# Kernel tuning notes

Hardware: AMD Instinct MI355X
Metric: run time of the kernel (lower is better)

Reference implementation:

```python
import jax, jax.numpy as jnp
import numpy as np

B, T, C, H = 2, 2048, 2048, 16
DH = C // H  # 128
INNER = 4 * C  # 8192
EPS = 1e-5


def _ln(x, w, b):
    mu = jnp.mean(x, axis=-1, keepdims=True)
    var = jnp.mean((x - mu) ** 2, axis=-1, keepdims=True)
    return (x - mu) * jax.lax.rsqrt(var + EPS) * w + b


def _apply_rotary(x, cos, sin):
    # x: [B,H,T,DH]; cos/sin: [T,DH//2] broadcast over B,H
    x1 = x[..., ::2]
    x2 = x[..., 1::2]
    r = jnp.stack([x1 * cos - x2 * sin, x1 * sin + x2 * cos], axis=-1)
    return r.reshape(r.shape[:-2] + (-1,))


def setup_inputs() -> dict:
    key = jax.random.key(0)
    ks = jax.random.split(key, 8)
    std = 0.02
    x = jax.random.normal(ks[0], (B, T, C), dtype=jnp.float32)
    # RoPE tables
    inv_freq = 1.0 / (10000.0 ** (np.arange(0, DH, 2, dtype=np.float32) / DH))
    ang = np.arange(T, dtype=np.float32)[:, None] * inv_freq[None, :]  # [T, DH//2]
    cos = jnp.asarray(np.cos(ang))
    sin = jnp.asarray(np.sin(ang))
    return {
        "x": x,
        "cos": cos,
        "sin": sin,
        "ln1_w": jnp.ones((C,), jnp.float32),
        "ln1_b": jnp.zeros((C,), jnp.float32),
        "ln2_w": jnp.ones((C,), jnp.float32),
        "ln2_b": jnp.zeros((C,), jnp.float32),
        "W_qkv": jax.random.normal(ks[1], (C, 3 * C), jnp.float32) * std,
        "W_o": jax.random.normal(ks[2], (C, C), jnp.float32) * std,
        "W1": jax.random.normal(ks[3], (C, INNER), jnp.float32) * std,
        "W2": jax.random.normal(ks[4], (C, INNER), jnp.float32) * std,
        "W3": jax.random.normal(ks[5], (INNER, C), jnp.float32) * std,
    }


def reference(x, cos, sin, ln1_w, ln1_b, ln2_w, ln2_b, W_qkv, W_o, W1, W2, W3):
    # --- attention sub-block (pre-LN) ---
    a = _ln(x, ln1_w, ln1_b)
    qkv = a @ W_qkv  # [B,T,3C]
    q, k, v = jnp.split(qkv, 3, axis=-1)
    q = q.reshape(B, T, H, DH).transpose(0, 2, 1, 3)  # [B,H,T,DH]
    k = k.reshape(B, T, H, DH).transpose(0, 2, 1, 3)
    v = v.reshape(B, T, H, DH).transpose(0, 2, 1, 3)
    q = _apply_rotary(q, cos, sin)
    k = _apply_rotary(k, cos, sin)
    scores = jnp.einsum("bhtd,bhsd->bhts", q, k) / jnp.sqrt(jnp.float32(DH))
    mask = jnp.triu(jnp.full((T, T), -jnp.inf, dtype=scores.dtype), k=1)
    scores = scores + mask
    attn = jax.nn.softmax(scores, axis=-1)
    y = jnp.einsum("bhts,bhsd->bhtd", attn, v)
    y = y.transpose(0, 2, 1, 3).reshape(B, T, C) @ W_o
    x = x + y
    # --- SwiGLU MLP sub-block (pre-LN) ---
    h = _ln(x, ln2_w, ln2_b)
    m = (jax.nn.silu(h @ W1) * (h @ W2)) @ W3
    return x + m
```

## Files before the change

kernel.cpp:

```cpp
#include <hip/hip_runtime.h>
#include <hip/hip_bf16.h>
#include <cstdint>

#define DEVINL __device__ __forceinline__

using f32x4  = __attribute__((ext_vector_type(4))) float;
using short8 = __attribute__((ext_vector_type(8))) short;
using short4v = __attribute__((ext_vector_type(4))) short;

DEVINL float bf2f(__hip_bfloat16 h){ return __bfloat162float(h); }
DEVINL __hip_bfloat16 f2bf(float f){ return __float2bfloat16(f); }
DEVINL short bfbits(float f){ __hip_bfloat16 h = __float2bfloat16(f); short s; __builtin_memcpy(&s, &h, 2); return s; }
DEVINL float sb2f(short s){ uint32_t u = ((uint32_t)(uint16_t)s) << 16; float f; __builtin_memcpy(&f, &u, 4); return f; }

DEVINL void gl_lds16(const void* g, void* l){
  __builtin_amdgcn_global_load_lds((const __attribute__((address_space(1))) void*)g,
                                   (__attribute__((address_space(3))) void*)l, 16, 0, 0);
}

__global__ __launch_bounds__(256) void wtrans(const float* __restrict__ src,
                                              __hip_bfloat16* __restrict__ dst,
                                              int R, int C){
  __shared__ float tile[32][33];
  const int tr0 = blockIdx.y*32, tc0 = blockIdx.x*32;
  const int t = threadIdx.x;
  const int lr = t >> 3, lc = (t & 7) * 4;
  float4 v = *(const float4*)(src + (size_t)(tr0+lr)*C + tc0 + lc);
  tile[lr][lc] = v.x; tile[lr][lc+1] = v.y; tile[lr][lc+2] = v.z; tile[lr][lc+3] = v.w;
  __syncthreads();
  short4v o;
  o[0] = bfbits(tile[lc+0][lr]);
  o[1] = bfbits(tile[lc+1][lr]);
  o[2] = bfbits(tile[lc+2][lr]);
  o[3] = bfbits(tile[lc+3][lr]);
  *(short4v*)(dst + (size_t)(tc0+lr)*R + tr0 + lc) = o;
}

__global__ __launch_bounds__(256) void ln_k(const float* __restrict__ x,
                                            const float* __restrict__ w,
                                            const float* __restrict__ bia,
                                            __hip_bfloat16* __restrict__ out){
  const int row = blockIdx.x, t = threadIdx.x;
  const float* xr = x + (size_t)row*2048;
  float4 v0 = *(const float4*)(xr + t*4);
  float4 v1 = *(const float4*)(xr + 1024 + t*4);
  float s  = v0.x+v0.y+v0.z+v0.w + v1.x+v1.y+v1.z+v1.w;
  float ss = v0.x*v0.x+v0.y*v0.y+v0.z*v0.z+v0.w*v0.w
           + v1.x*v1.x+v1.y*v1.y+v1.z*v1.z+v1.w*v1.w;
  #pragma unroll
  for (int o=1;o<64;o<<=1){ s += __shfl_xor(s,o); ss += __shfl_xor(ss,o); }
  __shared__ float red[8];
  const int wv = t>>6, ln = t&63;
  if (ln==0){ red[wv]=s; red[4+wv]=ss; }
  __syncthreads();
  s = red[0]+red[1]+red[2]+red[3]; ss = red[4]+red[5]+red[6]+red[7];
  const float mu = s*(1.f/2048.f);
  const float inv = rsqrtf(ss*(1.f/2048.f) - mu*mu + 1e-5f);
  {
    float4 wv4 = *(const float4*)(w + t*4);
    float4 bv4 = *(const float4*)(bia + t*4);
    short4v o;
    o[0]=bfbits((v0.x-mu)*inv*wv4.x + bv4.x);
    o[1]=bfbits((v0.y-mu)*inv*wv4.y + bv4.y);
    o[2]=bfbits((v0.z-mu)*inv*wv4.z + bv4.z);
    o[3]=bfbits((v0.w-mu)*inv*wv4.w + bv4.w);
    *(short4v*)(out + (size_t)row*2048 + t*4) = o;
  }
  {
    float4 wv4 = *(const float4*)(w + 1024 + t*4);
    float4 bv4 = *(const float4*)(bia + 1024 + t*4);
    short4v o;
    o[0]=bfbits((v1.x-mu)*inv*wv4.x + bv4.x);
    o[1]=bfbits((v1.y-mu)*inv*wv4.y + bv4.y);
    o[2]=bfbits((v1.z-mu)*inv*wv4.z + bv4.z);
    o[3]=bfbits((v1.w-mu)*inv*wv4.w + bv4.w);
    *(short4v*)(out + (size_t)row*2048 + 1024 + t*4) = o;
  }
}

template<int EPI, int BM>
__global__ __launch_bounds__(512, 2) void gemm256(
    const __hip_bfloat16* __restrict__ A,
    const __hip_bfloat16* __restrict__ Bt,
    __hip_bfloat16* __restrict__ Cb,
    float* __restrict__ Cf,
    const float* __restrict__ resid,
    const __hip_bfloat16* __restrict__ emul,
    int M, int N, int K, int NTN)
{
  constexpr int MF     = BM/32;
  constexpr int NA     = BM/64;
  constexpr int ABYTES = BM*128;
  constexpr int TILEB  = ABYTES + 32768;
  constexpr int NLD    = NA + 4;
  extern __shared__ char smem[];
  const int tid = threadIdx.x, lane = tid & 63, wave = tid >> 6;
  const int l15 = lane & 15, l4 = lane >> 4;
  const int wm = wave >> 2, wn = wave & 3;

  const int nwg = gridDim.x;
  const int id  = blockIdx.x;
  const int swz = (id & 7) * (nwg >> 3) + (id >> 3);
  const int by = swz / NTN, bx = swz % NTN;
  const int row0 = by * BM, col0 = bx * 256;

  const __hip_bfloat16* gptr[NLD];
  int ldsoff[NLD];
  #pragma unroll
  for (int g = 0; g < NLD; ++g){
    const int gg = (g < NA) ? g : g - NA;
    const int r    = gg*64 + (tid >> 3);
    const int colp = (tid & 7) * 16;
    const int coll = colp ^ ((r & 7) << 4);
    if (g < NA) gptr[g] = A  + (size_t)(row0 + r)*K + (coll >> 1);
    else        gptr[g] = Bt + (size_t)(col0 + r)*K + (coll >> 1);
    ldsoff[g] = (g < NA ? 0 : ABYTES) + gg*8192 + tid*16;
  }
  auto STAGE = [&](int bufc, int ktile){
    #pragma unroll
    for (int g = 0; g < NLD; ++g)
      gl_lds16(gptr[g] + (size_t)ktile*64, smem + bufc + ldsoff[g]);
  };

  const int swzm = (l15 & 7) << 4;
  const int aRow = (wm*(BM/2) + l15) * 128;
  const int bRow = ABYTES + (wn*64 + l15) * 128;
  const int colT0 = (l4*16) ^ swzm;
  const int colT1 = (64 + l4*16) ^ swzm;

  f32x4 acc[MF][4] = {};
  const int NT = K >> 6;

  STAGE(0, 0);
  STAGE(TILEB, 1);
  __builtin_amdgcn_sched_barrier(0);
  if constexpr (BM == 256) asm volatile("s_waitcnt vmcnt(8)" ::: "memory");
  else                     asm volatile("s_waitcnt vmcnt(6)" ::: "memory");
  __builtin_amdgcn_s_barrier();
  __builtin_amdgcn_sched_barrier(0);

  for (int t = 0; t < NT; ++t){
    const int bufc = (t & 1) * TILEB;
    #pragma unroll
    for (int ks = 0; ks < 2; ++ks){
      const int ct = (ks == 0) ? colT0 : colT1;
      short8 a[MF], b[4];
      #pragma unroll
      for (int m = 0; m < MF; ++m) a[m] = *(const short8*)(smem + bufc + aRow + m*2048 + ct);
      #pragma unroll
      for (int n = 0; n < 4; ++n) b[n] = *(const short8*)(smem + bufc + bRow + n*2048 + ct);
      __builtin_amdgcn_s_setprio(1);
      #pragma unroll
      for (int m = 0; m < MF; ++m)
        #pragma unroll
        for (int n = 0; n < 4; ++n)
          acc[m][n] = __builtin_amdgcn_mfma_f32_16x16x32_bf16(a[m], b[n], acc[m][n], 0, 0, 0);
      __builtin_amdgcn_s_setprio(0);
    }
    __builtin_amdgcn_sched_barrier(0);
    __builtin_amdgcn_s_barrier();
    __builtin_amdgcn_sched_barrier(0);
    if (t + 2 < NT){
      STAGE(bufc, t + 2);
      __builtin_amdgcn_sched_barrier(0);
      if constexpr (BM == 256) asm volatile("s_waitcnt vmcnt(8)" ::: "memory");
      else                     asm volatile("s_waitcnt vmcnt(6)" ::: "memory");
    } else {
      asm volatile("s_waitcnt vmcnt(0)" ::: "memory");
    }
    __builtin_amdgcn_s_barrier();
    __builtin_amdgcn_sched_barrier(0);
  }

  #pragma unroll
  for (int m = 0; m < MF; ++m){
    const int r0 = row0 + wm*(BM/2) + m*16 + l4*4;
    #pragma unroll
    for (int n = 0; n < 4; ++n){
      const int c = col0 + wn*64 + n*16 + l15;
      #pragma unroll
      for (int j = 0; j < 4; ++j){
        const size_t idx = (size_t)(r0 + j)*N + c;
        const float v = acc[m][n][j];
        if constexpr (EPI == 1)      Cf[idx] = v + resid[idx];
        else if constexpr (EPI == 2) Cb[idx] = f2bf(v / (1.f + __expf(-v)));
        else if constexpr (EPI == 3) Cb[idx] = f2bf(v * bf2f(emul[idx]));
        else                         Cb[idx] = f2bf(v);
      }
    }
  }
}

__global__ __launch_bounds__(256) void ropepack(
    const __hip_bfloat16* __restrict__ qkv, const float* __restrict__ cosT, const float* __restrict__ sinT,
    __hip_bfloat16* __restrict__ Qo, __hip_bfloat16* __restrict__ Ko, __hip_bfloat16* __restrict__ Vo)
{
  __shared__ short vt[128][72];
  const int bh = blockIdx.y, b = bh>>4, h = bh&15;
  const int t0 = blockIdx.x*64, tid = threadIdx.x;
  const int tr = tid>>2, q4 = tid&3;
  const int tg = t0 + tr;
  const __hip_bfloat16* base = qkv + ((size_t)(b*2048 + tg))*6144 + h*128;
  const int pp0 = q4*16;
  float cs[16], sn[16];
  #pragma unroll
  for (int i=0;i<4;i++){
    float4 c4 = *(const float4*)(cosT + (size_t)tg*64 + pp0 + i*4);
    float4 s4 = *(const float4*)(sinT + (size_t)tg*64 + pp0 + i*4);
    cs[i*4+0]=c4.x; cs[i*4+1]=c4.y; cs[i*4+2]=c4.z; cs[i*4+3]=c4.w;
    sn[i*4+0]=s4.x; sn[i*4+1]=s4.y; sn[i*4+2]=s4.z; sn[i*4+3]=s4.w;
  }
  #pragma unroll
  for (int qk=0; qk<2; ++qk){
    const __hip_bfloat16* src = base + qk*2048;
    __hip_bfloat16* dst = (qk==0 ? Qo : Ko) + ((size_t)bh*2048 + tg)*128 + pp0*2;
    short8 ov[4];
    short* o = (short*)ov;
    #pragma unroll
    for (int i=0;i<4;i++){
      short8 v = *(const short8*)(src + pp0*2 + i*8);
      #pragma unroll
      for (int j=0;j<4;j++){
        float xe = sb2f(v[2*j]), xo = sb2f(v[2*j+1]);
        float c = cs[4*i+j], s = sn[4*i+j];
        o[8*i+2*j]   = bfbits(xe*c - xo*s);
        o[8*i+2*j+1] = bfbits(xe*s + xo*c);
      }
    }
    #pragma unroll
    for (int i=0;i<4;i++) *(short8*)(dst + i*8) = ov[i];
  }
  const __hip_bfloat16* vsrc = base + 4096;
  const int vc0 = q4*32;
  #pragma unroll
  for (int i=0;i<4;i++){
    short8 v = *(const short8*)(vsrc + vc0 + i*8);
    #pragma unroll
    for (int j=0;j<8;j++) vt[vc0+i*8+j][tr] = v[j];
  }
  __syncthreads();
  const int d = tid>>1, th0 = (tid&1)*32;
  __hip_bfloat16* vdst = Vo + ((size_t)bh*128 + d)*2048 + t0 + th0;
  #pragma unroll
  for (int i=0;i<4;i++)
    *(short8*)(vdst + i*8) = *(const short8*)(&vt[d][th0 + i*8]);
}

__global__ __launch_bounds__(256) void attn_k(
    const __hip_bfloat16* __restrict__ Q,
    const __hip_bfloat16* __restrict__ K,
    const __hip_bfloat16* __restrict__ Vt,
    __hip_bfloat16* __restrict__ Y)
{
  __shared__ char lds[43008];
  const int bh = blockIdx.x, b = bh>>4, h = bh&15;
  const int by = blockIdx.y;
  const int qt = (by < 8) ? (15 - 2*by) : (2*(by - 8));
  const int tid = threadIdx.x, lane = tid&63, wave = tid>>6;
  const int qbase = qt*128 + wave*32;
  const int nsteps = qt*4 + 4;
  const __hip_bfloat16* Qh = Q + (size_t)bh*2048*128;
  const __hip_bfloat16* Kh = K + (size_t)bh*2048*128;
  const __hip_bfloat16* Vh = Vt + (size_t)bh*128*2048;
  __hip_bfloat16 (*pl)[40] = ((__hip_bfloat16 (*)[40])(lds + 32768)) + wave*32;
  const int l15 = lane & 15, l4 = lane >> 4;

  const int kr0 = tid >> 4, kj = tid & 15;
  const size_t ksrc0 = (size_t)kr0*128 + (((kj*16) ^ ((kr0 & 7) << 4)) >> 1);
  const int kr1 = kr0 + 16;
  const size_t ksrc1 = (size_t)kr1*128 + (((kj*16) ^ ((kr1 & 7) << 4)) >> 1);
  const int vd0 = tid >> 2, vj = tid & 3;
  const size_t vsrc0 = (size_t)vd0*2048 + vj*8;
  const size_t vsrc1 = (size_t)(vd0 + 64)*2048 + vj*8;
  auto STAGE = [&](int buf, int kv0){
    char* kb = lds + buf*8192 + tid*16;
    char* vb = lds + 16384 + buf*8192 + tid*16;
    gl_lds16(Kh + (size_t)kv0*128 + ksrc0, kb);
    gl_lds16(Kh + (size_t)kv0*128 + ksrc1, kb + 4096);
    gl_lds16(Vh + kv0 + vsrc0, vb);
    gl_lds16(Vh + kv0 + vsrc1, vb + 4096);
  };

  short8 qf[2][4];
  #pragma unroll
  for (int m=0;m<2;m++)
    #pragma unroll
    for (int kc=0;kc<4;kc++)
      qf[m][kc] = *(const short8*)(Qh + (size_t)(qbase + m*16 + l15)*128 + kc*32 + l4*8);

  f32x4 accO[2][8] = {};
  float mrow[2][4], lrow[2][4];
  #pragma unroll
  for (int m=0;m<2;m++)
    #pragma unroll
    for (int j=0;j<4;j++){ mrow[m][j] = -1e30f; lrow[m][j] = 0.f; }
  const float scale = 0.08838834764831845f;

  STAGE(0, 0);
  STAGE(1, 32);
  __builtin_amdgcn_sched_barrier(0);
  asm volatile("s_waitcnt vmcnt(4)" ::: "memory");
  __builtin_amdgcn_s_barrier();
  __builtin_amdgcn_sched_barrier(0);

  for (int s = 0; s < nsteps; ++s){
    const int kv0 = s*32;
    const char* kb = lds + (s&1)*8192;
    const char* vb = lds + 16384 + (s&1)*8192;
    if (kv0 <= qbase){
      const bool diag = (kv0 == qbase);
      short8 kf[8];
      #pragma unroll
      for (int n=0;n<2;n++)
        #pragma unroll
        for (int kc=0;kc<4;kc++)
          kf[n*4+kc] = *(const short8*)(kb + (n*16 + l15)*256 + ((kc*64 + l4*16) ^ ((l15 & 7) << 4)));
      f32x4 sc[2][2] = {};
      #pragma unroll
      for (int n=0;n<2;n++)
        #pragma unroll
        for (int m=0;m<2;m++)
          #pragma unroll
          for (int kc=0;kc<4;kc++)
            sc[m][n] = __builtin_amdgcn_mfma_f32_16x16x32_bf16(qf[m][kc], kf[n*4+kc], sc[m][n], 0,0,0);
      float alpha_[2][4];
      #pragma unroll
      for (int m=0;m<2;m++)
        #pragma unroll
        for (int j=0;j<4;j++){
          const int qr = 16*m + 4*l4 + j;
          float a0 = sc[m][0][j]*scale;
          float a1 = sc[m][1][j]*scale;
          if (diag){
            if (l15 > qr)      a0 = -1e30f;
            if (16 + l15 > qr) a1 = -1e30f;
          }
          float mx = fmaxf(a0, a1);
          #pragma unroll
          for (int o=1;o<16;o<<=1) mx = fmaxf(mx, __shfl_xor(mx, o));
          const float mn = fmaxf(mrow[m][j], mx);
          const float p0 = __expf(a0 - mn);
          const float p1 = __expf(a1 - mn);
          float sum = p0 + p1;
          #pragma unroll
          for (int o=1;o<16;o<<=1) sum += __shfl_xor(sum, o);
          const float al = __expf(mrow[m][j] - mn);
          lrow[m][j] = lrow[m][j]*al + sum;
          mrow[m][j] = mn;
          alpha_[m][j] = al;
          pl[qr][l15]    = f2bf(p0);
          pl[qr][16+l15] = f2bf(p1);
        }
      #pragma unroll
      for (int m=0;m<2;m++)
        #pragma unroll
        for (int db=0;db<8;db++)
          #pragma unroll
          for (int j=0;j<4;j++)
            accO[m][db][j] *= alpha_[m][j];
      asm volatile("s_waitcnt lgkmcnt(0)" ::: "memory");
      __builtin_amdgcn_sched_barrier(0);
      short8 pa[2];
      #pragma unroll
      for (int m=0;m<2;m++)
        pa[m] = *(const short8*)(&pl[m*16 + l15][l4*8]);
      short8 vf[8];
      #pragma unroll
      for (int db=0;db<8;db++)
        vf[db] = *(const short8*)(vb + (db*16 + l15)*64 + l4*16);
      #pragma unroll
      for (int db=0;db<8;db++)
        #pragma unroll
        for (int m=0;m<2;m++)
          accO[m][db] = __builtin_amdgcn_mfma_f32_16x16x32_bf16(pa[m], vf[db], accO[m][db], 0,0,0);
    }
    __builtin_amdgcn_sched_barrier(0);
    __builtin_amdgcn_s_barrier();
    __builtin_amdgcn_sched_barrier(0);
    if (s + 2 < nsteps){
      STAGE(s&1, (s+2)*32);
      __builtin_amdgcn_sched_barrier(0);
      asm volatile("s_waitcnt vmcnt(4)" ::: "memory");
    } else {
      asm volatile("s_waitcnt vmcnt(0)" ::: "memory");
    }
    __builtin_amdgcn_s_barrier();
    __builtin_amdgcn_sched_barrier(0);
  }

  #pragma unroll
  for (int m=0;m<2;m++)
    #pragma unroll
    for (int db=0;db<8;db++)
      #pragma unroll
      for (int j=0;j<4;j++){
        const int tg = qbase + 16*m + 4*l4 + j;
        const int d  = 16*db + l15;
        Y[((size_t)b*2048 + tg)*2048 + h*128 + d] = f2bf(accO[m][db][j] / lrow[m][j]);
      }
}

extern "C" void kernel_launch(void* const* d_in, const int* in_sizes, int n_in,
                              void* d_out, int out_size, void* d_ws, size_t ws_size,
                              hipStream_t stream)
{
  const float* x    = (const float*)d_in[0];
  const float* cosT = (const float*)d_in[1];
  const float* sinT = (const float*)d_in[2];
  const float* ln1w = (const float*)d_in[3];
  const float* ln1b = (const float*)d_in[4];
  const float* ln2w = (const float*)d_in[5];
  const float* ln2b = (const float*)d_in[6];
  const float* Wqkv = (const float*)d_in[7];
  const float* Wo   = (const float*)d_in[8];
  const float* W1   = (const float*)d_in[9];
  const float* W2   = (const float*)d_in[10];
  const float* W3   = (const float*)d_in[11];
  float* out = (float*)d_out;

  if (ws_size < 150994944) return;
  char* ws = (char*)d_ws;
  __hip_bfloat16* WT   = (__hip_bfloat16*)(ws);
  __hip_bfloat16* abf  = (__hip_bfloat16*)(ws + 33554432);
  __hip_bfloat16* qkvb = (__hip_bfloat16*)(ws + 50331648);
  __hip_bfloat16* Yb   = (__hip_bfloat16*)(ws + 50331648);
  __hip_bfloat16* sub  = (__hip_bfloat16*)(ws + 50331648);
  __hip_bfloat16* Qb   = (__hip_bfloat16*)(ws + 100663296);
  __hip_bfloat16* Kb   = (__hip_bfloat16*)(ws + 117440512);
  __hip_bfloat16* Vtb  = (__hip_bfloat16*)(ws + 134217728);
  float*          x2   = out;

  hipFuncSetAttribute(reinterpret_cast<const void*>(&gemm256<4,256>),
                      hipFuncAttributeMaxDynamicSharedMemorySize, 131072);
  hipFuncSetAttribute(reinterpret_cast<const void*>(&gemm256<2,256>),
                      hipFuncAttributeMaxDynamicSharedMemorySize, 131072);
  hipFuncSetAttribute(reinterpret_cast<const void*>(&gemm256<3,256>),
                      hipFuncAttributeMaxDynamicSharedMemorySize, 131072);
  hipFuncSetAttribute(reinterpret_cast<const void*>(&gemm256<1,128>),
                      hipFuncAttributeMaxDynamicSharedMemorySize, 98304);

  ln_k<<<4096,256,0,stream>>>(x, ln1w, ln1b, abf);
  wtrans<<<dim3(192,64),256,0,stream>>>(Wqkv, WT, 2048, 6144);
  gemm256<4,256><<<384,512,131072,stream>>>(abf, WT, qkvb, nullptr, nullptr, nullptr, 4096, 6144, 2048, 24);
  ropepack<<<dim3(32,32),256,0,stream>>>(qkvb, cosT, sinT, Qb, Kb, Vtb);
  attn_k<<<dim3(32,16),256,0,stream>>>(Qb, Kb, Vtb, Yb);
  wtrans<<<dim3(64,64),256,0,stream>>>(Wo, WT, 2048, 2048);
  gemm256<1,128><<<256,512,98304,stream>>>(Yb, WT, nullptr, x2, x, nullptr, 4096, 2048, 2048, 8);
  ln_k<<<4096,256,0,stream>>>(x2, ln2w, ln2b, abf);
  wtrans<<<dim3(256,64),256,0,stream>>>(W1, WT, 2048, 8192);
  gemm256<2,256><<<512,512,131072,stream>>>(abf, WT, sub, nullptr, nullptr, nullptr, 4096, 8192, 2048, 32);
  wtrans<<<dim3(256,64),256,0,stream>>>(W2, WT, 2048, 8192);
  gemm256<3,256><<<512,512,131072,stream>>>(abf, WT, sub, nullptr, nullptr, sub, 4096, 8192, 2048, 32);
  wtrans<<<dim3(64,256),256,0,stream>>>(W3, WT, 8192, 2048);
  gemm256<1,128><<<256,512,98304,stream>>>(sub, WT, nullptr, out, x2, nullptr, 4096, 2048, 8192, 8);
}
```

Measured before the change: 871.0 us.

## Pair causal query tiles per block, widen KV tile, compute row sums via MFMA

The attention kernel now runs 512 threads per block. Each block handles two complementary query tiles (qt and 15-qt), so causal work is balanced and each staged K/V tile is shared by 8 waves instead of 4. The KV step grows from 32 to 64 keys, and V is stored in LDS with a swizzled layout. The softmax row sum is no longer computed with shuffle reductions; an extra MFMA against a ones-column fragment produces it. Costs are larger dynamic LDS (100KB), more accumulator registers, and some wasted steps for the shorter tile's waves, which still sit through every barrier.

```diff
diff --git a/kernel.cpp b/kernel.cpp
--- a/kernel.cpp
+++ b/kernel.cpp
@@ -246,39 +246,41 @@
     *(short8*)(vdst + i*8) = *(const short8*)(&vt[d][th0 + i*8]);
 }
 
-__global__ __launch_bounds__(256) void attn_k(
+__global__ __launch_bounds__(512, 2) void attn_k(
     const __hip_bfloat16* __restrict__ Q,
     const __hip_bfloat16* __restrict__ K,
     const __hip_bfloat16* __restrict__ Vt,
     __hip_bfloat16* __restrict__ Y)
 {
-  __shared__ char lds[43008];
+  extern __shared__ char lds[];
   const int bh = blockIdx.x, b = bh>>4, h = bh&15;
   const int by = blockIdx.y;
-  const int qt = (by < 8) ? (15 - 2*by) : (2*(by - 8));
+  const int qtA = 15 - 2*by, qtB = 2*by;
   const int tid = threadIdx.x, lane = tid&63, wave = tid>>6;
-  const int qbase = qt*128 + wave*32;
-  const int nsteps = qt*4 + 4;
+  const int qt = (wave < 4) ? qtA : qtB;
+  const int qbase = qt*128 + (wave&3)*32;
+  const int qmax = (qtA > qtB) ? qtA : qtB;
+  const int nsteps = 2*qmax + 2;
   const __hip_bfloat16* Qh = Q + (size_t)bh*2048*128;
   const __hip_bfloat16* Kh = K + (size_t)bh*2048*128;
   const __hip_bfloat16* Vh = Vt + (size_t)bh*128*2048;
-  __hip_bfloat16 (*pl)[40] = ((__hip_bfloat16 (*)[40])(lds + 32768)) + wave*32;
+  char* plbase = lds + 65536 + wave*4608;
   const int l15 = lane & 15, l4 = lane >> 4;
-
-  const int kr0 = tid >> 4, kj = tid & 15;
-  const size_t ksrc0 = (size_t)kr0*128 + (((kj*16) ^ ((kr0 & 7) << 4)) >> 1);
-  const int kr1 = kr0 + 16;
-  const size_t ksrc1 = (size_t)kr1*128 + (((kj*16) ^ ((kr1 & 7) << 4)) >> 1);
-  const int vd0 = tid >> 2, vj = tid & 3;
-  const size_t vsrc0 = (size_t)vd0*2048 + vj*8;
-  const size_t vsrc1 = (size_t)(vd0 + 64)*2048 + vj*8;
+  const int swzm = (l15 & 7) << 4;
+
+  const int krA = tid >> 4;  const int kjA = (tid & 15) * 16;
+  const size_t ksrcA = (size_t)krA*128 + ((kjA ^ ((krA & 7) << 4)) >> 1);
+  const size_t ksrcB = (size_t)(krA+32)*128 + ((kjA ^ ((krA & 7) << 4)) >> 1);
+  const int vrA = tid >> 3;  const int vjA = (tid & 7) * 16;
+  const size_t vsrcA = (size_t)vrA*2048 + ((vjA ^ ((vrA & 7) << 4)) >> 1);
+  const size_t vsrcB = (size_t)(vrA+64)*2048 + ((vjA ^ ((vrA & 7) << 4)) >> 1);
   auto STAGE = [&](int buf, int kv0){
-    char* kb = lds + buf*8192 + tid*16;
-    char* vb = lds + 16384 + buf*8192 + tid*16;
-    gl_lds16(Kh + (size_t)kv0*128 + ksrc0, kb);
-    gl_lds16(Kh + (size_t)kv0*128 + ksrc1, kb + 4096);
-    gl_lds16(Vh + kv0 + vsrc0, vb);
-    gl_lds16(Vh + kv0 + vsrc1, vb + 4096);
+    char* kb = lds + buf*16384;
+    char* vb = lds + 32768 + buf*16384;
+    gl_lds16(Kh + (size_t)kv0*128 + ksrcA, kb + tid*16);
+    gl_lds16(Kh + (size_t)kv0*128 + ksrcB, kb + 8192 + tid*16);
+    gl_lds16(Vh + kv0 + vsrcA, vb + tid*16);
+    gl_lds16(Vh + kv0 + vsrcB, vb + 8192 + tid*16);
   };
 
   short8 qf[2][4];
@@ -288,97 +290,104 @@
     for (int kc=0;kc<4;kc++)
       qf[m][kc] = *(const short8*)(Qh + (size_t)(qbase + m*16 + l15)*128 + kc*32 + l4*8);
 
-  f32x4 accO[2][8] = {};
-  float mrow[2][4], lrow[2][4];
+  short8 of;
+  #pragma unroll
+  for (int i=0;i<8;i++) of[i] = (l15==0) ? (short)0x3F80 : (short)0;
+
+  f32x4 accO[2][9] = {};
+  float mrow[2][4];
   #pragma unroll
   for (int m=0;m<2;m++)
     #pragma unroll
-    for (int j=0;j<4;j++){ mrow[m][j] = -1e30f; lrow[m][j] = 0.f; }
+    for (int j=0;j<4;j++) mrow[m][j] = -1e30f;
   const float scale = 0.08838834764831845f;
 
   STAGE(0, 0);
-  STAGE(1, 32);
+  STAGE(1, 64);
   __builtin_amdgcn_sched_barrier(0);
   asm volatile("s_waitcnt vmcnt(4)" ::: "memory");
   __builtin_amdgcn_s_barrier();
   __builtin_amdgcn_sched_barrier(0);
 
   for (int s = 0; s < nsteps; ++s){
-    const int kv0 = s*32;
-    const char* kb = lds + (s&1)*8192;
-    const char* vb = lds + 16384 + (s&1)*8192;
+    const int kv0 = s*64;
+    const char* kb = lds + (s&1)*16384;
+    const char* vb = lds + 32768 + (s&1)*16384;
     if (kv0 <= qbase){
-      const bool diag = (kv0 == qbase);
-      short8 kf[8];
-      #pragma unroll
-      for (int n=0;n<2;n++)
+      const bool diag = (kv0 + 64 > qbase);
+      const int kvrel = kv0 - qbase;
+      f32x4 sc[2][4] = {};
+      #pragma unroll
+      for (int n=0;n<4;n++){
+        short8 kf[4];
         #pragma unroll
         for (int kc=0;kc<4;kc++)
-          kf[n*4+kc] = *(const short8*)(kb + (n*16 + l15)*256 + ((kc*64 + l4*16) ^ ((l15 & 7) << 4)));
-      f32x4 sc[2][2] = {};
-      #pragma unroll
-      for (int n=0;n<2;n++)
+          kf[kc] = *(const short8*)(kb + (n*16 + l15)*256 + ((kc*64 + l4*16) ^ swzm));
         #pragma unroll
         for (int m=0;m<2;m++)
           #pragma unroll
           for (int kc=0;kc<4;kc++)
-            sc[m][n] = __builtin_amdgcn_mfma_f32_16x16x32_bf16(qf[m][kc], kf[n*4+kc], sc[m][n], 0,0,0);
+            sc[m][n] = __builtin_amdgcn_mfma_f32_16x16x32_bf16(qf[m][kc], kf[kc], sc[m][n], 0,0,0);
+      }
       float alpha_[2][4];
       #pragma unroll
       for (int m=0;m<2;m++)
         #pragma unroll
         for (int j=0;j<4;j++){
           const int qr = 16*m + 4*l4 + j;
-          float a0 = sc[m][0][j]*scale;
-          float a1 = sc[m][1][j]*scale;
-          if (diag){
-            if (l15 > qr)      a0 = -1e30f;
-            if (16 + l15 > qr) a1 = -1e30f;
+          float a[4];
+          #pragma unroll
+          for (int n=0;n<4;n++){
+            a[n] = sc[m][n][j]*scale;
+            if (diag && (kvrel + n*16 + l15 > qr)) a[n] = -1e30f;
           }
-          float mx = fmaxf(a0, a1);
+          float mx = fmaxf(fmaxf(a[0],a[1]), fmaxf(a[2],a[3]));
           #pragma unroll
           for (int o=1;o<16;o<<=1) mx = fmaxf(mx, __shfl_xor(mx, o));
           const float mn = fmaxf(mrow[m][j], mx);
-          const float p0 = __expf(a0 - mn);
-          const float p1 = __expf(a1 - mn);
-          float sum = p0 + p1;
-          #pragma unroll
-          for (int o=1;o<16;o<<=1) sum += __shfl_xor(sum, o);
           const float al = __expf(mrow[m][j] - mn);
-          lrow[m][j] = lrow[m][j]*al + sum;
           mrow[m][j] = mn;
           alpha_[m][j] = al;
-          pl[qr][l15]    = f2bf(p0);
-          pl[qr][16+l15] = f2bf(p1);
+          __hip_bfloat16* pr = (__hip_bfloat16*)(plbase + qr*144) + l15;
+          #pragma unroll
+          for (int n=0;n<4;n++) pr[n*16] = f2bf(__expf(a[n] - mn));
         }
       #pragma unroll
       for (int m=0;m<2;m++)
         #pragma unroll
-        for (int db=0;db<8;db++)
+        for (int db=0;db<9;db++)
           #pragma unroll
           for (int j=0;j<4;j++)
             accO[m][db][j] *= alpha_[m][j];
       asm volatile("s_waitcnt lgkmcnt(0)" ::: "memory");
       __builtin_amdgcn_sched_barrier(0);
-      short8 pa[2];
+      short8 pa[2][2];
       #pragma unroll
       for (int m=0;m<2;m++)
-        pa[m] = *(const short8*)(&pl[m*16 + l15][l4*8]);
-      short8 vf[8];
-      #pragma unroll
-      for (int db=0;db<8;db++)
-        vf[db] = *(const short8*)(vb + (db*16 + l15)*64 + l4*16);
-      #pragma unroll
-      for (int db=0;db<8;db++)
+        #pragma unroll
+        for (int ks=0;ks<2;ks++)
+          pa[m][ks] = *(const short8*)(plbase + (m*16 + l15)*144 + ks*64 + l4*16);
+      #pragma unroll
+      for (int db=0;db<8;db++){
+        #pragma unroll
+        for (int ks=0;ks<2;ks++){
+          short8 vf = *(const short8*)(vb + (db*16 + l15)*128 + ((ks*64 + l4*16) ^ swzm));
+          #pragma unroll
+          for (int m=0;m<2;m++)
+            accO[m][db] = __builtin_amdgcn_mfma_f32_16x16x32_bf16(pa[m][ks], vf, accO[m][db], 0,0,0);
+        }
+      }
+      #pragma unroll
+      for (int ks=0;ks<2;ks++)
         #pragma unroll
         for (int m=0;m<2;m++)
-          accO[m][db] = __builtin_amdgcn_mfma_f32_16x16x32_bf16(pa[m], vf[db], accO[m][db], 0,0,0);
+          accO[m][8] = __builtin_amdgcn_mfma_f32_16x16x32_bf16(pa[m][ks], of, accO[m][8], 0,0,0);
     }
     __builtin_amdgcn_sched_barrier(0);
     __builtin_amdgcn_s_barrier();
     __builtin_amdgcn_sched_barrier(0);
     if (s + 2 < nsteps){
-      STAGE(s&1, (s+2)*32);
+      STAGE(s&1, (s+2)*64);
       __builtin_amdgcn_sched_barrier(0);
       asm volatile("s_waitcnt vmcnt(4)" ::: "memory");
     } else {
@@ -389,15 +398,19 @@
   }
 
   #pragma unroll
-  for (int m=0;m<2;m++)
+  for (int m=0;m<2;m++){
+    float lr[4];
+    #pragma unroll
+    for (int j=0;j<4;j++) lr[j] = __shfl(accO[m][8][j], l4*16);
     #pragma unroll
     for (int db=0;db<8;db++)
       #pragma unroll
       for (int j=0;j<4;j++){
         const int tg = qbase + 16*m + 4*l4 + j;
         const int d  = 16*db + l15;
-        Y[((size_t)b*2048 + tg)*2048 + h*128 + d] = f2bf(accO[m][db][j] / lrow[m][j]);
+        Y[((size_t)b*2048 + tg)*2048 + h*128 + d] = f2bf(accO[m][db][j] / lr[j]);
       }
+  }
 }
 
 extern "C" void kernel_launch(void* const* d_in, const int* in_sizes, int n_in,
@@ -438,12 +451,14 @@
                       hipFuncAttributeMaxDynamicSharedMemorySize, 131072);
   hipFuncSetAttribute(reinterpret_cast<const void*>(&gemm256<1,128>),
                       hipFuncAttributeMaxDynamicSharedMemorySize, 98304);
+  hipFuncSetAttribute(reinterpret_cast<const void*>(&attn_k),
+                      hipFuncAttributeMaxDynamicSharedMemorySize, 102400);
 
   ln_k<<<4096,256,0,stream>>>(x, ln1w, ln1b, abf);
   wtrans<<<dim3(192,64),256,0,stream>>>(Wqkv, WT, 2048, 6144);
   gemm256<4,256><<<384,512,131072,stream>>>(abf, WT, qkvb, nullptr, nullptr, nullptr, 4096, 6144, 2048, 24);
   ropepack<<<dim3(32,32),256,0,stream>>>(qkvb, cosT, sinT, Qb, Kb, Vtb);
-  attn_k<<<dim3(32,16),256,0,stream>>>(Qb, Kb, Vtb, Yb);
+  attn_k<<<dim3(32,8),512,102400,stream>>>(Qb, Kb, Vtb, Yb);
   wtrans<<<dim3(64,64),256,0,stream>>>(Wo, WT, 2048, 2048);
   gemm256<1,128><<<256,512,98304,stream>>>(Yb, WT, nullptr, x2, x, nullptr, 4096, 2048, 2048, 8);
   ln_k<<<4096,256,0,stream>>>(x2, ln2w, ln2b, abf);
```

Result: faster. 813.3 us (-6.6%).
